# Kernel optimization log

Hardware: AMD Instinct MI355X
Metric: run time of the kernel (lower is better)

Reference implementation:

```python
import jax, jax.numpy as jnp
import numpy as np

B, T, C = 2, 4096, 768
H = 12
D = C // H  # head_dim = 64


def setup_inputs() -> dict:
    key = jax.random.key(0)
    k1, k2, k3 = jax.random.split(key, 3)
    x = jax.random.normal(k1, (B, T, C), dtype=jnp.float32)
    Wqkv = jax.random.normal(k2, (C, 3 * C), dtype=jnp.float32) * (C ** -0.5)
    Wproj = jax.random.normal(k3, (C, C), dtype=jnp.float32) * (C ** -0.5)
    bproj = jnp.zeros((C,), dtype=jnp.float32)
    return {"x": x, "Wqkv": Wqkv, "Wproj": Wproj, "bproj": bproj}


def reference(x, Wqkv, Wproj, bproj):
    b, t, c = x.shape
    # qkv projection (no bias), split into heads: [3, B, H, T, D]
    qkv = (x @ Wqkv).reshape(b, t, 3, H, D).transpose(2, 0, 3, 1, 4)
    q, k, v = qkv[0], qkv[1], qkv[2]
    scale = D ** -0.5
    # full causal score matrix [B, H, T, T] (faithful to naive impl)
    scores = jnp.einsum('bhqd,bhkd->bhqk', q, k) * scale
    causal = jnp.tril(jnp.ones((t, t), dtype=bool))
    scores = jnp.where(causal[None, None], scores, -jnp.inf)
    attn = jax.nn.softmax(scores, axis=-1)
    out = jnp.einsum('bhqk,bhkd->bhqd', attn, v)
    out = out.transpose(0, 2, 1, 3).reshape(b, t, c)
    return out @ Wproj + bproj
```

## Files before the change

### kernel.cpp

```cpp
#include <hip/hip_runtime.h>

#define B_ 2
#define T_ 4096
#define C_ 768
#define H_ 12
#define D_ 64
#define QTASK 96

typedef __attribute__((ext_vector_type(8))) short bf16x8;
typedef __attribute__((ext_vector_type(4))) float f32x4;
typedef __attribute__((ext_vector_type(16))) float f32x16;

__device__ __forceinline__ unsigned short f2bf(float f) {
  union { float f; unsigned u; } v; v.f = f;
  unsigned r = v.u + 0x7fffu + ((v.u >> 16) & 1u);
  return (unsigned short)(r >> 16);
}

__device__ __forceinline__ float exp2_hw(float x) {
  float r;
  asm("v_exp_f32 %0, %1" : "=v"(r) : "v"(x));
  return r;
}

__device__ __forceinline__ void gll16(const void* g, void* l) {
  __builtin_amdgcn_global_load_lds((const __attribute__((address_space(1))) void*)g,
                                   (__attribute__((address_space(3))) void*)l, 16, 0, 0);
}


__global__ __launch_bounds__(256) void cast_bf16_k(const float* __restrict__ in,
                                                   unsigned short* __restrict__ out, int n4,
                                                   unsigned* __restrict__ cnt) {
  int i = blockIdx.x * 256 + threadIdx.x;
  if (i < 128) cnt[i] = 0u;
  if (i >= n4) return;
  float4 v = ((const float4*)in)[i];
  union { unsigned short s[4]; unsigned long long u; } o;
  o.s[0] = f2bf(v.x); o.s[1] = f2bf(v.y); o.s[2] = f2bf(v.z); o.s[3] = f2bf(v.w);
  ((unsigned long long*)out)[i] = o.u;
}

__global__ __launch_bounds__(256) void tpose_cast_k(const float* __restrict__ in,
                                                    unsigned short* __restrict__ out,
                                                    int R, int C) {
  __shared__ unsigned short t[64][65];
  const int c0 = blockIdx.x * 64, r0 = blockIdx.y * 64;
  const int tr = threadIdx.x >> 6, tc = threadIdx.x & 63;
#pragma unroll
  for (int i = 0; i < 16; ++i) {
    int r = i * 4 + tr;
    t[r][tc] = f2bf(in[(size_t)(r0 + r) * C + c0 + tc]);
  }
  __syncthreads();
#pragma unroll
  for (int i = 0; i < 16; ++i) {
    int c = i * 4 + tr;
    out[(size_t)(c0 + c) * R + r0 + tc] = t[tc][c];
  }
}


#define QSCALE 0.1803368801111243f

template <int MODE>
__global__ __launch_bounds__(256) void gemm_k(const unsigned short* __restrict__ A,
                                              const unsigned short* __restrict__ Bt,
                                              int K,
                                              unsigned short* __restrict__ q_out,
                                              unsigned short* __restrict__ k_out,
                                              unsigned short* __restrict__ vt_out,
                                              float* __restrict__ f_out,
                                              const float* __restrict__ bias) {
  __shared__ short a_lds[2][128 * 32];
  __shared__ short b_lds[2][128 * 32];
  const int tid = threadIdx.x;
  const int wave = tid >> 6, lane = tid & 63;
  const int wm = wave >> 1, wn = wave & 1;
  const int lr = lane & 15, lc = lane >> 4;

  const int id = blockIdx.x;
  const int xcd = id & 7, idc = id >> 3;
  const int bx = xcd * 8 + (idc & 7);
  const int by = idc >> 3;
  const int m0 = bx * 128, n0 = by * 128;

  f32x4 acc[4][4];
  for (int mi = 0; mi < 4; ++mi)
    for (int ni = 0; ni < 4; ++ni) acc[mi][ni] = (f32x4){0.f, 0.f, 0.f, 0.f};

  const unsigned short *ap[2], *bp[2];
  int lb[2];
#pragma unroll
  for (int p = 0; p < 2; ++p) {
    int chunk = p * 256 + wave * 64 + lane;
    int r = chunk >> 2, cc = chunk & 3;
    int c = cc ^ ((r >> 1) & 3);
    ap[p] = A + (size_t)(m0 + r) * K + c * 8;
    bp[p] = Bt + (size_t)(n0 + r) * K + c * 8;
    lb[p] = (p * 256 + wave * 64) * 8;
  }

  const int nks = K >> 5;
#pragma unroll
  for (int p = 0; p < 2; ++p) {
    gll16(ap[p], &a_lds[0][lb[p]]);
    gll16(bp[p], &b_lds[0][lb[p]]);
    ap[p] += 32; bp[p] += 32;
  }

  for (int ks = 0; ks < nks; ++ks) {
    const int buf = ks & 1;
    __builtin_amdgcn_s_barrier();
    __builtin_amdgcn_sched_barrier(0);
    if (ks + 1 < nks) {
#pragma unroll
      for (int p = 0; p < 2; ++p) {
        gll16(ap[p], &a_lds[buf ^ 1][lb[p]]);
        gll16(bp[p], &b_lds[buf ^ 1][lb[p]]);
        ap[p] += 32; bp[p] += 32;
      }
      asm volatile("s_waitcnt vmcnt(4)" ::: "memory");
    } else {
      asm volatile("s_waitcnt vmcnt(0)" ::: "memory");
    }
    __builtin_amdgcn_sched_barrier(0);
    __builtin_amdgcn_s_barrier();
    __builtin_amdgcn_sched_barrier(0);

    bf16x8 af[4], bfrag[4];
#pragma unroll
    for (int mi = 0; mi < 4; ++mi) {
      int r = wm * 64 + mi * 16 + lr;
      af[mi] = *(const bf16x8*)&a_lds[buf][r * 32 + (lc ^ ((r >> 1) & 3)) * 8];
    }
#pragma unroll
    for (int ni = 0; ni < 4; ++ni) {
      int r = wn * 64 + ni * 16 + lr;
      bfrag[ni] = *(const bf16x8*)&b_lds[buf][r * 32 + (lc ^ ((r >> 1) & 3)) * 8];
    }
    __builtin_amdgcn_s_setprio(1);
#pragma unroll
    for (int mi = 0; mi < 4; ++mi)
#pragma unroll
      for (int ni = 0; ni < 4; ++ni)
        acc[mi][ni] = __builtin_amdgcn_mfma_f32_16x16x32_bf16(af[mi], bfrag[ni], acc[mi][ni], 0, 0, 0);
    __builtin_amdgcn_s_setprio(0);
  }

  if (MODE == 0) {
    const int nn0 = n0 + wn * 64 + lr;
    const int which = n0 / 768;
#pragma unroll
    for (int mi = 0; mi < 4; ++mi)
#pragma unroll
      for (int ni = 0; ni < 4; ++ni) {
        int nn = nn0 + ni * 16;
        int rem = nn - which * 768;
        int h = rem >> 6, d = rem & 63;
        int t0v = m0 + wm * 64 + mi * 16 + lc * 4;
        int b = t0v >> 12, t = t0v & (T_ - 1);
        size_t bh = (size_t)(b * H_ + h);
        if (which == 2) {
          unsigned u0, u1;
          asm("v_cvt_pk_bf16_f32 %0, %1, %2" : "=v"(u0) : "v"(acc[mi][ni][0]), "v"(acc[mi][ni][1]));
          asm("v_cvt_pk_bf16_f32 %0, %1, %2" : "=v"(u1) : "v"(acc[mi][ni][2]), "v"(acc[mi][ni][3]));
          uint2 u = {u0, u1};
          *(uint2*)&vt_out[(bh * D_ + d) * T_ + t] = u;
        } else {
#pragma unroll
          for (int r = 0; r < 4; ++r) {
            float av = acc[mi][ni][r];
            if (which == 0) av *= QSCALE;
            unsigned short val = f2bf(av);
            if (which == 0) q_out[(bh * T_ + t + r) * D_ + d] = val;
            else            k_out[(bh * T_ + t + r) * D_ + d] = val;
          }
        }
      }
  } else {
#pragma unroll
    for (int mi = 0; mi < 4; ++mi)
#pragma unroll
      for (int ni = 0; ni < 4; ++ni) {
        int nn = n0 + wn * 64 + ni * 16 + lr;
        float bv = bias[nn];
#pragma unroll
        for (int r = 0; r < 4; ++r) {
          int m = m0 + wm * 64 + mi * 16 + lc * 4 + r;
          f_out[(size_t)m * C_ + nn] = acc[mi][ni][r] + bv;
        }
      }
  }
}


#define PACK8(SV, O)                                                              \
  do {                                                                            \
    unsigned w0, w1, w2, w3, w4, w5, w6, w7;                                      \
    asm("v_cvt_pk_bf16_f32 %0, %1, %2" : "=v"(w0) : "v"(SV[0]), "v"(SV[1]));      \
    asm("v_cvt_pk_bf16_f32 %0, %1, %2" : "=v"(w1) : "v"(SV[2]), "v"(SV[3]));      \
    asm("v_cvt_pk_bf16_f32 %0, %1, %2" : "=v"(w2) : "v"(SV[4]), "v"(SV[5]));      \
    asm("v_cvt_pk_bf16_f32 %0, %1, %2" : "=v"(w3) : "v"(SV[6]), "v"(SV[7]));      \
    asm("v_cvt_pk_bf16_f32 %0, %1, %2" : "=v"(w4) : "v"(SV[8]), "v"(SV[9]));      \
    asm("v_cvt_pk_bf16_f32 %0, %1, %2" : "=v"(w5) : "v"(SV[10]), "v"(SV[11]));    \
    asm("v_cvt_pk_bf16_f32 %0, %1, %2" : "=v"(w6) : "v"(SV[12]), "v"(SV[13]));    \
    asm("v_cvt_pk_bf16_f32 %0, %1, %2" : "=v"(w7) : "v"(SV[14]), "v"(SV[15]));    \
    asm("v_permlane32_swap_b32 %0, %1" : "+v"(w0), "+v"(w2));                     \
    asm("v_permlane32_swap_b32 %0, %1" : "+v"(w1), "+v"(w3));                     \
    asm("v_permlane32_swap_b32 %0, %1" : "+v"(w4), "+v"(w6));                     \
    asm("v_permlane32_swap_b32 %0, %1" : "+v"(w5), "+v"(w7));                     \
    pw[(O) + 0] = w0; pw[(O) + 1] = w1; pw[(O) + 2] = w2; pw[(O) + 3] = w3;       \
    pw[(O) + 4] = w4; pw[(O) + 5] = w5; pw[(O) + 6] = w6; pw[(O) + 7] = w7;       \
  } while (0)

__global__ __launch_bounds__(256) void flash5_k(const unsigned short* __restrict__ Qg,
                                                const unsigned short* __restrict__ Kg,
                                                const unsigned short* __restrict__ Vtg,
                                                unsigned short* __restrict__ Og,
                                                unsigned* __restrict__ cnt) {
  __shared__ short k_lds[2][8 * 512];
  __shared__ short vt_lds[2][8 * 512];
  __shared__ int task_s;

  const int tid = threadIdx.x;
  const int wave = tid >> 6, lane = tid & 63;
  const int lq = lane & 31, hi = lane >> 5;
  const int xq = blockIdx.x & 7;
  unsigned* myq = cnt + xq * 16;

  for (;;) {
    if (tid == 0) task_s = (int)atomicAdd(myq, 1u);
    __syncthreads();
    const int task = task_s;
    if (task >= QTASK) return;

    const int qi = 31 - task / 3;
    const int bh = xq * 3 + (task - (task / 3) * 3);
    const int qw = qi * 128 + wave * 32;
    const int q_g = qw + lq;

    const size_t kbase = (size_t)bh * T_ * D_;
    const size_t vbase = (size_t)bh * D_ * T_;

    const unsigned short* qrow = Qg + kbase + (size_t)q_g * D_;
    bf16x8 qf[4];
#pragma unroll
    for (int t = 0; t < 4; ++t) qf[t] = *(const bf16x8*)(qrow + t * 16 + hi * 8);

    f32x16 accT0, accT1;
#pragma unroll
    for (int r = 0; r < 16; ++r) { accT0[r] = 0.f; accT1[r] = 0.f; }
    float lvec[16];
#pragma unroll
    for (int r = 0; r < 16; ++r) lvec[r] = 0.f;
    float m = 0.f;

    const int nt = 2 * qi + 2;

    const unsigned short* kp = Kg + kbase + (size_t)((wave & 1) * 32 + lq) * D_ + (wave >> 1) * 16 + hi * 8;
    const unsigned short* vp = Vtg + vbase + (size_t)((wave & 1) * 32 + lq) * T_ + (wave >> 1) * 16 + hi * 8;
    const int lb0 = wave * 512, lb1 = (wave + 4) * 512;

    gll16(kp, &k_lds[0][lb0]); gll16(kp + 32, &k_lds[0][lb1]);
    gll16(vp, &vt_lds[0][lb0]); gll16(vp + 32, &vt_lds[0][lb1]);
    const unsigned short* kpn = kp + 64 * D_;
    const unsigned short* vpn = vp + 64;

    for (int it = 0; it < nt; ++it) {
      const int kv = it * 64;
      const int buf = it & 1;

      __builtin_amdgcn_s_barrier();
      __builtin_amdgcn_sched_barrier(0);
      if (it + 1 < nt) {
        gll16(kpn, &k_lds[buf ^ 1][lb0]); gll16(kpn + 32, &k_lds[buf ^ 1][lb1]);
        gll16(vpn, &vt_lds[buf ^ 1][lb0]); gll16(vpn + 32, &vt_lds[buf ^ 1][lb1]);
        kpn += 64 * D_; vpn += 64;
        asm volatile("s_waitcnt vmcnt(4)" ::: "memory");
      } else {
        asm volatile("s_waitcnt vmcnt(0)" ::: "memory");
      }
      __builtin_amdgcn_sched_barrier(0);
      __builtin_amdgcn_s_barrier();
      __builtin_amdgcn_sched_barrier(0);

      if (kv <= qw + 31) {
        const float negm = -m;
        f32x16 s0, s1;
#pragma unroll
        for (int r = 0; r < 16; ++r) { s0[r] = negm; s1[r] = negm; }
        __builtin_amdgcn_s_setprio(1);
#pragma unroll
        for (int t = 0; t < 4; ++t) {
          bf16x8 kf0 = *(const bf16x8*)&k_lds[buf][(t * 2 + 0) * 512 + lane * 8];
          bf16x8 kf1 = *(const bf16x8*)&k_lds[buf][(t * 2 + 1) * 512 + lane * 8];
          s0 = __builtin_amdgcn_mfma_f32_32x32x16_bf16(kf0, qf[t], s0, 0, 0, 0);
          s1 = __builtin_amdgcn_mfma_f32_32x32x16_bf16(kf1, qf[t], s1, 0, 0, 0);
        }
        __builtin_amdgcn_s_setprio(0);

        if (kv + 63 > qw) {
#pragma unroll
          for (int r = 0; r < 16; ++r) {
            int key0 = kv + ((r & 3) + 8 * (r >> 2) + 4 * hi);
            if (key0 > q_g) s0[r] = -INFINITY;
            if (key0 + 32 > q_g) s1[r] = -INFINITY;
          }
        }

        float mx[16];
#pragma unroll
        for (int r = 0; r < 16; ++r) mx[r] = fmaxf(s0[r], s1[r]);
        float a0 = fmaxf(fmaxf(mx[0], mx[1]), mx[2]);
        float a1 = fmaxf(fmaxf(mx[3], mx[4]), mx[5]);
        float a2 = fmaxf(fmaxf(mx[6], mx[7]), mx[8]);
        float a3 = fmaxf(fmaxf(mx[9], mx[10]), mx[11]);
        float a4 = fmaxf(fmaxf(mx[12], mx[13]), mx[14]);
        float rx = fmaxf(fmaxf(fmaxf(a0, a1), fmaxf(a2, a3)), fmaxf(a4, mx[15]));
        rx = fmaxf(rx, __shfl_xor(rx, 32));

        if (!__all(rx <= 8.f)) {
          float dlt = fmaxf(rx, 0.f);
          float al = exp2_hw(-dlt);
          m += dlt;
#pragma unroll
          for (int r = 0; r < 16; ++r) { accT0[r] *= al; accT1[r] *= al; lvec[r] *= al; }
#pragma unroll
          for (int r = 0; r < 16; ++r) { s0[r] -= dlt; s1[r] -= dlt; }
        }
#pragma unroll
        for (int r = 0; r < 16; ++r) s0[r] = exp2_hw(s0[r]);
#pragma unroll
        for (int r = 0; r < 16; ++r) s1[r] = exp2_hw(s1[r]);
#pragma unroll
        for (int r = 0; r < 16; ++r) lvec[r] += s0[r] + s1[r];

        unsigned pw[16];
        PACK8(s0, 0);
        PACK8(s1, 8);

        __builtin_amdgcn_s_setprio(1);
#pragma unroll
        for (int ks = 0; ks < 4; ++ks) {
          union { unsigned u[4]; bf16x8 v; } pb;
          pb.u[0] = pw[ks * 4 + 0]; pb.u[1] = pw[ks * 4 + 1];
          pb.u[2] = pw[ks * 4 + 2]; pb.u[3] = pw[ks * 4 + 3];
          bf16x8 vf0 = *(const bf16x8*)&vt_lds[buf][(ks * 2 + 0) * 512 + lane * 8];
          bf16x8 vf1 = *(const bf16x8*)&vt_lds[buf][(ks * 2 + 1) * 512 + lane * 8];
          accT0 = __builtin_amdgcn_mfma_f32_32x32x16_bf16(vf0, pb.v, accT0, 0, 0, 0);
          accT1 = __builtin_amdgcn_mfma_f32_32x32x16_bf16(vf1, pb.v, accT1, 0, 0, 0);
        }
        __builtin_amdgcn_s_setprio(0);
      }
    }

    float l = 0.f;
#pragma unroll
    for (int r = 0; r < 16; ++r) l += lvec[r];
    l += __shfl_xor(l, 32);
    const float inv = 1.0f / l;
    const int b = bh / H_, h = bh - b * H_;
    unsigned short* orow = Og + ((size_t)b * T_ + q_g) * C_ + h * D_;
#pragma unroll
    for (int g = 0; g < 4; ++g) {
      int d0 = 8 * g + 4 * hi;
      float e0 = accT0[4 * g + 0] * inv, e1 = accT0[4 * g + 1] * inv;
      float e2 = accT0[4 * g + 2] * inv, e3 = accT0[4 * g + 3] * inv;
      float f0 = accT1[4 * g + 0] * inv, f1 = accT1[4 * g + 1] * inv;
      float f2 = accT1[4 * g + 2] * inv, f3 = accT1[4 * g + 3] * inv;
      uint2 ua, ub;
      asm("v_cvt_pk_bf16_f32 %0, %1, %2" : "=v"(ua.x) : "v"(e0), "v"(e1));
      asm("v_cvt_pk_bf16_f32 %0, %1, %2" : "=v"(ua.y) : "v"(e2), "v"(e3));
      asm("v_cvt_pk_bf16_f32 %0, %1, %2" : "=v"(ub.x) : "v"(f0), "v"(f1));
      asm("v_cvt_pk_bf16_f32 %0, %1, %2" : "=v"(ub.y) : "v"(f2), "v"(f3));
      *(uint2*)(orow + d0) = ua;
      *(uint2*)(orow + 32 + d0) = ub;
    }
    __syncthreads();
  }
}


extern "C" void kernel_launch(void* const* d_in, const int* in_sizes, int n_in,
                              void* d_out, int out_size, void* d_ws, size_t ws_size,
                              hipStream_t stream) {
  const float* x     = (const float*)d_in[0];
  const float* Wqkv  = (const float*)d_in[1];
  const float* Wproj = (const float*)d_in[2];
  const float* bproj = (const float*)d_in[3];
  float* out = (float*)d_out;

  char* ws = (char*)d_ws;
  unsigned short* xbf   = (unsigned short*)(ws);
  unsigned short* wqkvt = (unsigned short*)(ws + 12582912);
  unsigned short* wprjt = (unsigned short*)(ws + 16121856);
  unsigned short* Qb    = (unsigned short*)(ws + 17301504);
  unsigned short* Kb    = (unsigned short*)(ws + 29884416);
  unsigned short* Vtb   = (unsigned short*)(ws + 42467328);
  unsigned*       cnt   = (unsigned*)(ws + 55050240);

  cast_bf16_k<<<6144, 256, 0, stream>>>(x, xbf, (B_ * T_ * C_) / 4, cnt);
  tpose_cast_k<<<dim3((3 * C_) / 64, C_ / 64), 256, 0, stream>>>(Wqkv, wqkvt, C_, 3 * C_);
  tpose_cast_k<<<dim3(C_ / 64, C_ / 64), 256, 0, stream>>>(Wproj, wprjt, C_, C_);

  gemm_k<0><<<(B_ * T_ / 128) * (3 * C_ / 128), 256, 0, stream>>>(
      xbf, wqkvt, C_, Qb, Kb, Vtb, nullptr, nullptr);

  flash5_k<<<1024, 256, 0, stream>>>(Qb, Kb, Vtb, xbf, cnt);

  gemm_k<1><<<(B_ * T_ / 128) * (C_ / 128), 256, 0, stream>>>(
      xbf, wprjt, C_, nullptr, nullptr, nullptr, out, bproj);
}
```

Baseline: 197.5 us.

## Split long causal query tiles across two workgroups with ticketed partial merge

The flash-attention kernel now splits the 16 longest causal query tiles of each head into two halves along the key range. Each half is processed by a separate task. The first finisher writes bf16 partial accumulators plus its (m, l) to workspace. The second, identified by an atomic ticket, merges both with a log-sum-exp rescale and writes the output. A task table interleaves split and unsplit tiles so the work per task is more even, reducing the tail imbalance of the longest tiles. The cost is extra global traffic, an acquire/release atomic per split tile, and bf16 rounding of the partial accumulators.

```diff
diff --git a/kernel.cpp b/kernel.cpp
--- a/kernel.cpp
+++ b/kernel.cpp
@@ -5,7 +5,7 @@
 #define C_ 768
 #define H_ 12
 #define D_ 64
-#define QTASK 96
+#define QTASK 144
 
 typedef __attribute__((ext_vector_type(8))) short bf16x8;
 typedef __attribute__((ext_vector_type(4))) float f32x4;
@@ -33,7 +33,7 @@
                                                    unsigned short* __restrict__ out, int n4,
                                                    unsigned* __restrict__ cnt) {
   int i = blockIdx.x * 256 + threadIdx.x;
-  if (i < 128) cnt[i] = 0u;
+  if (i < 512) cnt[i] = 0u;
   if (i >= n4) return;
   float4 v = ((const float4*)in)[i];
   union { unsigned short s[4]; unsigned long long u; } o;
@@ -194,6 +194,25 @@
   }
 }
 
+__device__ const unsigned char g_tasktbl[48] = {
+  15, 0x80|31, 0xC0|31,
+      0x80|30, 0xC0|30,
+  14, 0x80|29, 0xC0|29,
+      0x80|28, 0xC0|28,
+  13, 0x80|27, 0xC0|27,
+      0x80|26, 0xC0|26,
+  12, 0x80|25, 0xC0|25,
+      0x80|24, 0xC0|24,
+  11, 0x80|23, 0xC0|23,
+      0x80|22, 0xC0|22,
+  10, 0x80|21, 0xC0|21,
+      0x80|20, 0xC0|20,
+   9, 0x80|19, 0xC0|19,
+      0x80|18, 0xC0|18,
+   8, 0x80|17, 0xC0|17,
+      0x80|16, 0xC0|16,
+   7, 6, 5, 4, 3, 2, 1, 0
+};
 
 #define PACK8(SV, O)                                                              \
   do {                                                                            \
@@ -214,14 +233,17 @@
     pw[(O) + 4] = w4; pw[(O) + 5] = w5; pw[(O) + 6] = w6; pw[(O) + 7] = w7;       \
   } while (0)
 
-__global__ __launch_bounds__(256) void flash5_k(const unsigned short* __restrict__ Qg,
+__global__ __launch_bounds__(256) void flash6_k(const unsigned short* __restrict__ Qg,
                                                 const unsigned short* __restrict__ Kg,
                                                 const unsigned short* __restrict__ Vtg,
                                                 unsigned short* __restrict__ Og,
-                                                unsigned* __restrict__ cnt) {
+                                                unsigned* __restrict__ cnt,
+                                                unsigned* __restrict__ tickets,
+                                                unsigned short* __restrict__ partials) {
   __shared__ short k_lds[2][8 * 512];
   __shared__ short vt_lds[2][8 * 512];
   __shared__ int task_s;
+  __shared__ int tk_s;
 
   const int tid = threadIdx.x;
   const int wave = tid >> 6, lane = tid & 63;
@@ -235,11 +257,19 @@
     const int task = task_s;
     if (task >= QTASK) return;
 
-    const int qi = 31 - task / 3;
-    const int bh = xq * 3 + (task - (task / 3) * 3);
+    const int d3 = task / 3;
+    const int desc = g_tasktbl[d3];
+    const int qi = desc & 63;
+    const int split = desc >> 7;
+    const int half = (desc >> 6) & 1;
+    const int bh = xq * 3 + (task - d3 * 3);
     const int qw = qi * 128 + wave * 32;
     const int q_g = qw + lq;
 
+    const int it0 = (split && half) ? (qi + 1) : 0;
+    const int itN = split ? (half ? (2 * qi + 2) : (qi + 1)) : (2 * qi + 2);
+    const int ntl = itN - it0;
+
     const size_t kbase = (size_t)bh * T_ * D_;
     const size_t vbase = (size_t)bh * D_ * T_;
 
@@ -256,10 +286,10 @@
     for (int r = 0; r < 16; ++r) lvec[r] = 0.f;
     float m = 0.f;
 
-    const int nt = 2 * qi + 2;
-
-    const unsigned short* kp = Kg + kbase + (size_t)((wave & 1) * 32 + lq) * D_ + (wave >> 1) * 16 + hi * 8;
-    const unsigned short* vp = Vtg + vbase + (size_t)((wave & 1) * 32 + lq) * T_ + (wave >> 1) * 16 + hi * 8;
+    const unsigned short* kp = Kg + kbase + (size_t)((wave & 1) * 32 + lq) * D_ +
+                               (wave >> 1) * 16 + hi * 8 + (size_t)it0 * 64 * D_;
+    const unsigned short* vp = Vtg + vbase + (size_t)((wave & 1) * 32 + lq) * T_ +
+                               (wave >> 1) * 16 + hi * 8 + it0 * 64;
     const int lb0 = wave * 512, lb1 = (wave + 4) * 512;
 
     gll16(kp, &k_lds[0][lb0]); gll16(kp + 32, &k_lds[0][lb1]);
@@ -267,13 +297,13 @@
     const unsigned short* kpn = kp + 64 * D_;
     const unsigned short* vpn = vp + 64;
 
-    for (int it = 0; it < nt; ++it) {
-      const int kv = it * 64;
-      const int buf = it & 1;
+    for (int j = 0; j < ntl; ++j) {
+      const int kv = (it0 + j) * 64;
+      const int buf = j & 1;
 
       __builtin_amdgcn_s_barrier();
       __builtin_amdgcn_sched_barrier(0);
-      if (it + 1 < nt) {
+      if (j + 1 < ntl) {
         gll16(kpn, &k_lds[buf ^ 1][lb0]); gll16(kpn + 32, &k_lds[buf ^ 1][lb1]);
         gll16(vpn, &vt_lds[buf ^ 1][lb0]); gll16(vpn + 32, &vt_lds[buf ^ 1][lb1]);
         kpn += 64 * D_; vpn += 64;
@@ -359,23 +389,92 @@
 #pragma unroll
     for (int r = 0; r < 16; ++r) l += lvec[r];
     l += __shfl_xor(l, 32);
-    const float inv = 1.0f / l;
-    const int b = bh / H_, h = bh - b * H_;
-    unsigned short* orow = Og + ((size_t)b * T_ + q_g) * C_ + h * D_;
-#pragma unroll
-    for (int g = 0; g < 4; ++g) {
-      int d0 = 8 * g + 4 * hi;
-      float e0 = accT0[4 * g + 0] * inv, e1 = accT0[4 * g + 1] * inv;
-      float e2 = accT0[4 * g + 2] * inv, e3 = accT0[4 * g + 3] * inv;
-      float f0 = accT1[4 * g + 0] * inv, f1 = accT1[4 * g + 1] * inv;
-      float f2 = accT1[4 * g + 2] * inv, f3 = accT1[4 * g + 3] * inv;
-      uint2 ua, ub;
-      asm("v_cvt_pk_bf16_f32 %0, %1, %2" : "=v"(ua.x) : "v"(e0), "v"(e1));
-      asm("v_cvt_pk_bf16_f32 %0, %1, %2" : "=v"(ua.y) : "v"(e2), "v"(e3));
-      asm("v_cvt_pk_bf16_f32 %0, %1, %2" : "=v"(ub.x) : "v"(f0), "v"(f1));
-      asm("v_cvt_pk_bf16_f32 %0, %1, %2" : "=v"(ub.y) : "v"(f2), "v"(f3));
-      *(uint2*)(orow + d0) = ua;
-      *(uint2*)(orow + 32 + d0) = ub;
+
+    bool do_write = true;
+    if (split) {
+      const int slot = bh * 16 + (qi - 16);
+      const int sub = slot * 2 + half;
+      unsigned short* pb = partials + (size_t)sub * 9216;
+      {
+        unsigned w[16];
+#pragma unroll
+        for (int g = 0; g < 8; ++g)
+          asm("v_cvt_pk_bf16_f32 %0, %1, %2" : "=v"(w[g]) : "v"(accT0[2 * g]), "v"(accT0[2 * g + 1]));
+#pragma unroll
+        for (int g = 0; g < 8; ++g)
+          asm("v_cvt_pk_bf16_f32 %0, %1, %2" : "=v"(w[8 + g]) : "v"(accT1[2 * g]), "v"(accT1[2 * g + 1]));
+        uint4* po = (uint4*)(pb + tid * 32);
+#pragma unroll
+        for (int g = 0; g < 4; ++g) {
+          uint4 u = {w[4 * g + 0], w[4 * g + 1], w[4 * g + 2], w[4 * g + 3]};
+          po[g] = u;
+        }
+        float2* pml = (float2*)(pb + 8192);
+        float2 ml = {m, l};
+        pml[tid] = ml;
+      }
+      __syncthreads();
+      if (tid == 0)
+        tk_s = (int)__hip_atomic_fetch_add(&tickets[slot], 1u, __ATOMIC_ACQ_REL,
+                                           __HIP_MEMORY_SCOPE_AGENT);
+      __syncthreads();
+      if (tk_s == 0) {
+        do_write = false;
+      } else {
+        const unsigned short* pb2 = partials + (size_t)(slot * 2 + (half ^ 1)) * 9216;
+        float2 oml = ((const float2*)(pb2 + 8192))[tid];
+        float newm = fmaxf(m, oml.x);
+        float se = exp2_hw(m - newm), so = exp2_hw(oml.x - newm);
+        l = l * se + oml.y * so;
+        const uint4* pv = (const uint4*)(pb2 + tid * 32);
+#pragma unroll
+        for (int g = 0; g < 2; ++g) {
+          uint4 u = pv[g];
+#pragma unroll
+          for (int e = 0; e < 4; ++e) {
+            unsigned wv = ((const unsigned*)&u)[e];
+            union { unsigned u; float f; } flo, fhi;
+            flo.u = wv << 16; fhi.u = wv & 0xffff0000u;
+            int r = g * 8 + e * 2;
+            accT0[r] = accT0[r] * se + flo.f * so;
+            accT0[r + 1] = accT0[r + 1] * se + fhi.f * so;
+          }
+        }
+#pragma unroll
+        for (int g = 0; g < 2; ++g) {
+          uint4 u = pv[2 + g];
+#pragma unroll
+          for (int e = 0; e < 4; ++e) {
+            unsigned wv = ((const unsigned*)&u)[e];
+            union { unsigned u; float f; } flo, fhi;
+            flo.u = wv << 16; fhi.u = wv & 0xffff0000u;
+            int r = g * 8 + e * 2;
+            accT1[r] = accT1[r] * se + flo.f * so;
+            accT1[r + 1] = accT1[r + 1] * se + fhi.f * so;
+          }
+        }
+      }
+    }
+
+    if (do_write) {
+      const float inv = 1.0f / l;
+      const int b = bh / H_, h = bh - b * H_;
+      unsigned short* orow = Og + ((size_t)b * T_ + q_g) * C_ + h * D_;
+#pragma unroll
+      for (int g = 0; g < 4; ++g) {
+        int d0 = 8 * g + 4 * hi;
+        float e0 = accT0[4 * g + 0] * inv, e1 = accT0[4 * g + 1] * inv;
+        float e2 = accT0[4 * g + 2] * inv, e3 = accT0[4 * g + 3] * inv;
+        float f0 = accT1[4 * g + 0] * inv, f1 = accT1[4 * g + 1] * inv;
+        float f2 = accT1[4 * g + 2] * inv, f3 = accT1[4 * g + 3] * inv;
+        uint2 ua, ub;
+        asm("v_cvt_pk_bf16_f32 %0, %1, %2" : "=v"(ua.x) : "v"(e0), "v"(e1));
+        asm("v_cvt_pk_bf16_f32 %0, %1, %2" : "=v"(ua.y) : "v"(e2), "v"(e3));
+        asm("v_cvt_pk_bf16_f32 %0, %1, %2" : "=v"(ub.x) : "v"(f0), "v"(f1));
+        asm("v_cvt_pk_bf16_f32 %0, %1, %2" : "=v"(ub.y) : "v"(f2), "v"(f3));
+        *(uint2*)(orow + d0) = ua;
+        *(uint2*)(orow + 32 + d0) = ub;
+      }
     }
     __syncthreads();
   }
@@ -399,6 +498,8 @@
   unsigned short* Kb    = (unsigned short*)(ws + 29884416);
   unsigned short* Vtb   = (unsigned short*)(ws + 42467328);
   unsigned*       cnt   = (unsigned*)(ws + 55050240);
+  unsigned*       tick  = (unsigned*)(ws + 55050240 + 512);
+  unsigned short* part  = (unsigned short*)(ws + 55052288);
 
   cast_bf16_k<<<6144, 256, 0, stream>>>(x, xbf, (B_ * T_ * C_) / 4, cnt);
   tpose_cast_k<<<dim3((3 * C_) / 64, C_ / 64), 256, 0, stream>>>(Wqkv, wqkvt, C_, 3 * C_);
@@ -407,7 +508,7 @@
   gemm_k<0><<<(B_ * T_ / 128) * (3 * C_ / 128), 256, 0, stream>>>(
       xbf, wqkvt, C_, Qb, Kb, Vtb, nullptr, nullptr);
 
-  flash5_k<<<1024, 256, 0, stream>>>(Qb, Kb, Vtb, xbf, cnt);
+  flash6_k<<<1024, 256, 0, stream>>>(Qb, Kb, Vtb, xbf, cnt, tick, part);
 
   gemm_k<1><<<(B_ * T_ / 128) * (C_ / 128), 256, 0, stream>>>(
       xbf, wprjt, C_, nullptr, nullptr, nullptr, out, bproj);
```

Measured after the change: 212.6 us. 1.08x slower.

## Replace atomic task queue flash kernel with static-grid per-wave direct-load attention

Applied to the files above, without the earlier changes.

Rewrites the attention kernel to drop the atomic work-queue and the shared LDS double-buffering. Each wave now loads its K and V fragments straight from global memory into registers and loops only over its own causal key tiles, so there are no block barriers. Blocks are statically assigned, with query tiles interleaved long and short to balance load, and occupancy is hinted at 3 blocks. The cost is that K/V reuse across the four waves now relies on cache rather than LDS, and global-load latency is no longer hidden by an explicit prefetch.

```diff
diff --git a/kernel.cpp b/kernel.cpp
--- a/kernel.cpp
+++ b/kernel.cpp
@@ -5,7 +5,6 @@
 #define C_ 768
 #define H_ 12
 #define D_ 64
-#define QTASK 96
 
 typedef __attribute__((ext_vector_type(8))) short bf16x8;
 typedef __attribute__((ext_vector_type(4))) float f32x4;
@@ -30,10 +29,8 @@
 
 
 __global__ __launch_bounds__(256) void cast_bf16_k(const float* __restrict__ in,
-                                                   unsigned short* __restrict__ out, int n4,
-                                                   unsigned* __restrict__ cnt) {
+                                                   unsigned short* __restrict__ out, int n4) {
   int i = blockIdx.x * 256 + threadIdx.x;
-  if (i < 128) cnt[i] = 0u;
   if (i >= n4) return;
   float4 v = ((const float4*)in)[i];
   union { unsigned short s[4]; unsigned long long u; } o;
@@ -214,170 +211,144 @@
     pw[(O) + 4] = w4; pw[(O) + 5] = w5; pw[(O) + 6] = w6; pw[(O) + 7] = w7;       \
   } while (0)
 
-__global__ __launch_bounds__(256) void flash5_k(const unsigned short* __restrict__ Qg,
-                                                const unsigned short* __restrict__ Kg,
-                                                const unsigned short* __restrict__ Vtg,
-                                                unsigned short* __restrict__ Og,
-                                                unsigned* __restrict__ cnt) {
-  __shared__ short k_lds[2][8 * 512];
-  __shared__ short vt_lds[2][8 * 512];
-  __shared__ int task_s;
-
+__global__ __launch_bounds__(256, 3) void flash7_k(const unsigned short* __restrict__ Qg,
+                                                   const unsigned short* __restrict__ Kg,
+                                                   const unsigned short* __restrict__ Vtg,
+                                                   unsigned short* __restrict__ Og) {
   const int tid = threadIdx.x;
   const int wave = tid >> 6, lane = tid & 63;
   const int lq = lane & 31, hi = lane >> 5;
-  const int xq = blockIdx.x & 7;
-  unsigned* myq = cnt + xq * 16;
-
-  for (;;) {
-    if (tid == 0) task_s = (int)atomicAdd(myq, 1u);
-    __syncthreads();
-    const int task = task_s;
-    if (task >= QTASK) return;
-
-    const int qi = 31 - task / 3;
-    const int bh = xq * 3 + (task - (task / 3) * 3);
-    const int qw = qi * 128 + wave * 32;
-    const int q_g = qw + lq;
-
-    const size_t kbase = (size_t)bh * T_ * D_;
-    const size_t vbase = (size_t)bh * D_ * T_;
-
-    const unsigned short* qrow = Qg + kbase + (size_t)q_g * D_;
-    bf16x8 qf[4];
-#pragma unroll
-    for (int t = 0; t < 4; ++t) qf[t] = *(const bf16x8*)(qrow + t * 16 + hi * 8);
-
-    f32x16 accT0, accT1;
-#pragma unroll
-    for (int r = 0; r < 16; ++r) { accT0[r] = 0.f; accT1[r] = 0.f; }
-    float lvec[16];
-#pragma unroll
-    for (int r = 0; r < 16; ++r) lvec[r] = 0.f;
-    float m = 0.f;
-
-    const int nt = 2 * qi + 2;
-
-    const unsigned short* kp = Kg + kbase + (size_t)((wave & 1) * 32 + lq) * D_ + (wave >> 1) * 16 + hi * 8;
-    const unsigned short* vp = Vtg + vbase + (size_t)((wave & 1) * 32 + lq) * T_ + (wave >> 1) * 16 + hi * 8;
-    const int lb0 = wave * 512, lb1 = (wave + 4) * 512;
-
-    gll16(kp, &k_lds[0][lb0]); gll16(kp + 32, &k_lds[0][lb1]);
-    gll16(vp, &vt_lds[0][lb0]); gll16(vp + 32, &vt_lds[0][lb1]);
-    const unsigned short* kpn = kp + 64 * D_;
-    const unsigned short* vpn = vp + 64;
-
-    for (int it = 0; it < nt; ++it) {
-      const int kv = it * 64;
-      const int buf = it & 1;
-
-      __builtin_amdgcn_s_barrier();
-      __builtin_amdgcn_sched_barrier(0);
-      if (it + 1 < nt) {
-        gll16(kpn, &k_lds[buf ^ 1][lb0]); gll16(kpn + 32, &k_lds[buf ^ 1][lb1]);
-        gll16(vpn, &vt_lds[buf ^ 1][lb0]); gll16(vpn + 32, &vt_lds[buf ^ 1][lb1]);
-        kpn += 64 * D_; vpn += 64;
-        asm volatile("s_waitcnt vmcnt(4)" ::: "memory");
-      } else {
-        asm volatile("s_waitcnt vmcnt(0)" ::: "memory");
+
+  const int bid = blockIdx.x;
+  const int xcd = bid & 7, j = bid >> 3;
+  const int g = j / 3, rb = j - g * 3;
+  const int bh = xcd * 3 + rb;
+  const int qi = (g & 1) ? (g >> 1) : (31 - (g >> 1));
+
+  const int qw = qi * 128 + wave * 32;
+  const int q_g = qw + lq;
+  const int ntw = (qw >> 6) + 1;
+
+  const size_t kbase = (size_t)bh * T_ * D_;
+  const size_t vbase = (size_t)bh * D_ * T_;
+
+  const unsigned short* qrow = Qg + kbase + (size_t)q_g * D_;
+  bf16x8 qf[4];
+#pragma unroll
+  for (int t = 0; t < 4; ++t) qf[t] = *(const bf16x8*)(qrow + t * 16 + hi * 8);
+
+  f32x16 accT0, accT1;
+#pragma unroll
+  for (int r = 0; r < 16; ++r) { accT0[r] = 0.f; accT1[r] = 0.f; }
+  float lvec[8];
+#pragma unroll
+  for (int r = 0; r < 8; ++r) lvec[r] = 0.f;
+  float m = 0.f;
+
+  const unsigned short* kp0 = Kg + kbase + (size_t)lq * D_ + hi * 8;
+  const unsigned short* vp0 = Vtg + vbase + (size_t)lq * T_ + hi * 8;
+
+  for (int it = 0; it < ntw; ++it) {
+    const int kv = it * 64;
+    const unsigned short* kp = kp0 + (size_t)kv * D_;
+    const unsigned short* vp = vp0 + kv;
+
+    bf16x8 kf[8], vf[8];
+#pragma unroll
+    for (int t = 0; t < 4; ++t) {
+      kf[2 * t]     = *(const bf16x8*)(kp + t * 16);
+      kf[2 * t + 1] = *(const bf16x8*)(kp + 32 * D_ + t * 16);
+      vf[2 * t]     = *(const bf16x8*)(vp + t * 16);
+      vf[2 * t + 1] = *(const bf16x8*)(vp + (size_t)32 * T_ + t * 16);
+    }
+
+    const float negm = -m;
+    f32x16 s0, s1;
+#pragma unroll
+    for (int r = 0; r < 16; ++r) { s0[r] = negm; s1[r] = negm; }
+    __builtin_amdgcn_s_setprio(1);
+#pragma unroll
+    for (int t = 0; t < 4; ++t) {
+      s0 = __builtin_amdgcn_mfma_f32_32x32x16_bf16(kf[2 * t], qf[t], s0, 0, 0, 0);
+      s1 = __builtin_amdgcn_mfma_f32_32x32x16_bf16(kf[2 * t + 1], qf[t], s1, 0, 0, 0);
+    }
+    __builtin_amdgcn_s_setprio(0);
+
+    if (kv + 63 > qw) {
+#pragma unroll
+      for (int r = 0; r < 16; ++r) {
+        int key0 = kv + ((r & 3) + 8 * (r >> 2) + 4 * hi);
+        if (key0 > q_g) s0[r] = -INFINITY;
+        if (key0 + 32 > q_g) s1[r] = -INFINITY;
       }
-      __builtin_amdgcn_sched_barrier(0);
-      __builtin_amdgcn_s_barrier();
-      __builtin_amdgcn_sched_barrier(0);
-
-      if (kv <= qw + 31) {
-        const float negm = -m;
-        f32x16 s0, s1;
-#pragma unroll
-        for (int r = 0; r < 16; ++r) { s0[r] = negm; s1[r] = negm; }
-        __builtin_amdgcn_s_setprio(1);
-#pragma unroll
-        for (int t = 0; t < 4; ++t) {
-          bf16x8 kf0 = *(const bf16x8*)&k_lds[buf][(t * 2 + 0) * 512 + lane * 8];
-          bf16x8 kf1 = *(const bf16x8*)&k_lds[buf][(t * 2 + 1) * 512 + lane * 8];
-          s0 = __builtin_amdgcn_mfma_f32_32x32x16_bf16(kf0, qf[t], s0, 0, 0, 0);
-          s1 = __builtin_amdgcn_mfma_f32_32x32x16_bf16(kf1, qf[t], s1, 0, 0, 0);
-        }
-        __builtin_amdgcn_s_setprio(0);
-
-        if (kv + 63 > qw) {
-#pragma unroll
-          for (int r = 0; r < 16; ++r) {
-            int key0 = kv + ((r & 3) + 8 * (r >> 2) + 4 * hi);
-            if (key0 > q_g) s0[r] = -INFINITY;
-            if (key0 + 32 > q_g) s1[r] = -INFINITY;
-          }
-        }
-
-        float mx[16];
-#pragma unroll
-        for (int r = 0; r < 16; ++r) mx[r] = fmaxf(s0[r], s1[r]);
-        float a0 = fmaxf(fmaxf(mx[0], mx[1]), mx[2]);
-        float a1 = fmaxf(fmaxf(mx[3], mx[4]), mx[5]);
-        float a2 = fmaxf(fmaxf(mx[6], mx[7]), mx[8]);
-        float a3 = fmaxf(fmaxf(mx[9], mx[10]), mx[11]);
-        float a4 = fmaxf(fmaxf(mx[12], mx[13]), mx[14]);
-        float rx = fmaxf(fmaxf(fmaxf(a0, a1), fmaxf(a2, a3)), fmaxf(a4, mx[15]));
-        rx = fmaxf(rx, __shfl_xor(rx, 32));
-
-        if (!__all(rx <= 8.f)) {
-          float dlt = fmaxf(rx, 0.f);
-          float al = exp2_hw(-dlt);
-          m += dlt;
-#pragma unroll
-          for (int r = 0; r < 16; ++r) { accT0[r] *= al; accT1[r] *= al; lvec[r] *= al; }
-#pragma unroll
-          for (int r = 0; r < 16; ++r) { s0[r] -= dlt; s1[r] -= dlt; }
-        }
-#pragma unroll
-        for (int r = 0; r < 16; ++r) s0[r] = exp2_hw(s0[r]);
-#pragma unroll
-        for (int r = 0; r < 16; ++r) s1[r] = exp2_hw(s1[r]);
-#pragma unroll
-        for (int r = 0; r < 16; ++r) lvec[r] += s0[r] + s1[r];
-
-        unsigned pw[16];
-        PACK8(s0, 0);
-        PACK8(s1, 8);
-
-        __builtin_amdgcn_s_setprio(1);
-#pragma unroll
-        for (int ks = 0; ks < 4; ++ks) {
-          union { unsigned u[4]; bf16x8 v; } pb;
-          pb.u[0] = pw[ks * 4 + 0]; pb.u[1] = pw[ks * 4 + 1];
-          pb.u[2] = pw[ks * 4 + 2]; pb.u[3] = pw[ks * 4 + 3];
-          bf16x8 vf0 = *(const bf16x8*)&vt_lds[buf][(ks * 2 + 0) * 512 + lane * 8];
-          bf16x8 vf1 = *(const bf16x8*)&vt_lds[buf][(ks * 2 + 1) * 512 + lane * 8];
-          accT0 = __builtin_amdgcn_mfma_f32_32x32x16_bf16(vf0, pb.v, accT0, 0, 0, 0);
-          accT1 = __builtin_amdgcn_mfma_f32_32x32x16_bf16(vf1, pb.v, accT1, 0, 0, 0);
-        }
-        __builtin_amdgcn_s_setprio(0);
-      }
-    }
-
-    float l = 0.f;
-#pragma unroll
-    for (int r = 0; r < 16; ++r) l += lvec[r];
-    l += __shfl_xor(l, 32);
-    const float inv = 1.0f / l;
-    const int b = bh / H_, h = bh - b * H_;
-    unsigned short* orow = Og + ((size_t)b * T_ + q_g) * C_ + h * D_;
-#pragma unroll
-    for (int g = 0; g < 4; ++g) {
-      int d0 = 8 * g + 4 * hi;
-      float e0 = accT0[4 * g + 0] * inv, e1 = accT0[4 * g + 1] * inv;
-      float e2 = accT0[4 * g + 2] * inv, e3 = accT0[4 * g + 3] * inv;
-      float f0 = accT1[4 * g + 0] * inv, f1 = accT1[4 * g + 1] * inv;
-      float f2 = accT1[4 * g + 2] * inv, f3 = accT1[4 * g + 3] * inv;
-      uint2 ua, ub;
-      asm("v_cvt_pk_bf16_f32 %0, %1, %2" : "=v"(ua.x) : "v"(e0), "v"(e1));
-      asm("v_cvt_pk_bf16_f32 %0, %1, %2" : "=v"(ua.y) : "v"(e2), "v"(e3));
-      asm("v_cvt_pk_bf16_f32 %0, %1, %2" : "=v"(ub.x) : "v"(f0), "v"(f1));
-      asm("v_cvt_pk_bf16_f32 %0, %1, %2" : "=v"(ub.y) : "v"(f2), "v"(f3));
-      *(uint2*)(orow + d0) = ua;
-      *(uint2*)(orow + 32 + d0) = ub;
-    }
-    __syncthreads();
+    }
+
+    float mx[16];
+#pragma unroll
+    for (int r = 0; r < 16; ++r) mx[r] = fmaxf(s0[r], s1[r]);
+    float a0 = fmaxf(fmaxf(mx[0], mx[1]), mx[2]);
+    float a1 = fmaxf(fmaxf(mx[3], mx[4]), mx[5]);
+    float a2 = fmaxf(fmaxf(mx[6], mx[7]), mx[8]);
+    float a3 = fmaxf(fmaxf(mx[9], mx[10]), mx[11]);
+    float a4 = fmaxf(fmaxf(mx[12], mx[13]), mx[14]);
+    float rx = fmaxf(fmaxf(fmaxf(a0, a1), fmaxf(a2, a3)), fmaxf(a4, mx[15]));
+    rx = fmaxf(rx, __shfl_xor(rx, 32));
+
+    if (!__all(rx <= 8.f)) {
+      float dlt = fmaxf(rx, 0.f);
+      float al = exp2_hw(-dlt);
+      m += dlt;
+#pragma unroll
+      for (int r = 0; r < 16; ++r) { accT0[r] *= al; accT1[r] *= al; }
+#pragma unroll
+      for (int r = 0; r < 8; ++r) lvec[r] *= al;
+#pragma unroll
+      for (int r = 0; r < 16; ++r) { s0[r] -= dlt; s1[r] -= dlt; }
+    }
+#pragma unroll
+    for (int r = 0; r < 16; ++r) s0[r] = exp2_hw(s0[r]);
+#pragma unroll
+    for (int r = 0; r < 16; ++r) s1[r] = exp2_hw(s1[r]);
+#pragma unroll
+    for (int r = 0; r < 8; ++r) lvec[r] += (s0[r] + s1[r]) + (s0[r + 8] + s1[r + 8]);
+
+    unsigned pw[16];
+    PACK8(s0, 0);
+    PACK8(s1, 8);
+
+    __builtin_amdgcn_s_setprio(1);
+#pragma unroll
+    for (int ks = 0; ks < 4; ++ks) {
+      union { unsigned u[4]; bf16x8 v; } pb;
+      pb.u[0] = pw[ks * 4 + 0]; pb.u[1] = pw[ks * 4 + 1];
+      pb.u[2] = pw[ks * 4 + 2]; pb.u[3] = pw[ks * 4 + 3];
+      accT0 = __builtin_amdgcn_mfma_f32_32x32x16_bf16(vf[2 * ks], pb.v, accT0, 0, 0, 0);
+      accT1 = __builtin_amdgcn_mfma_f32_32x32x16_bf16(vf[2 * ks + 1], pb.v, accT1, 0, 0, 0);
+    }
+    __builtin_amdgcn_s_setprio(0);
+  }
+
+  float l = 0.f;
+#pragma unroll
+  for (int r = 0; r < 8; ++r) l += lvec[r];
+  l += __shfl_xor(l, 32);
+  const float inv = 1.0f / l;
+  const int b = bh / H_, h = bh - b * H_;
+  unsigned short* orow = Og + ((size_t)b * T_ + q_g) * C_ + h * D_;
+#pragma unroll
+  for (int gg = 0; gg < 4; ++gg) {
+    int d0 = 8 * gg + 4 * hi;
+    float e0 = accT0[4 * gg + 0] * inv, e1 = accT0[4 * gg + 1] * inv;
+    float e2 = accT0[4 * gg + 2] * inv, e3 = accT0[4 * gg + 3] * inv;
+    float f0 = accT1[4 * gg + 0] * inv, f1 = accT1[4 * gg + 1] * inv;
+    float f2 = accT1[4 * gg + 2] * inv, f3 = accT1[4 * gg + 3] * inv;
+    uint2 ua, ub;
+    asm("v_cvt_pk_bf16_f32 %0, %1, %2" : "=v"(ua.x) : "v"(e0), "v"(e1));
+    asm("v_cvt_pk_bf16_f32 %0, %1, %2" : "=v"(ua.y) : "v"(e2), "v"(e3));
+    asm("v_cvt_pk_bf16_f32 %0, %1, %2" : "=v"(ub.x) : "v"(f0), "v"(f1));
+    asm("v_cvt_pk_bf16_f32 %0, %1, %2" : "=v"(ub.y) : "v"(f2), "v"(f3));
+    *(uint2*)(orow + d0) = ua;
+    *(uint2*)(orow + 32 + d0) = ub;
   }
 }
 
@@ -398,16 +369,15 @@
   unsigned short* Qb    = (unsigned short*)(ws + 17301504);
   unsigned short* Kb    = (unsigned short*)(ws + 29884416);
   unsigned short* Vtb   = (unsigned short*)(ws + 42467328);
-  unsigned*       cnt   = (unsigned*)(ws + 55050240);
-
-  cast_bf16_k<<<6144, 256, 0, stream>>>(x, xbf, (B_ * T_ * C_) / 4, cnt);
+
+  cast_bf16_k<<<6144, 256, 0, stream>>>(x, xbf, (B_ * T_ * C_) / 4);
   tpose_cast_k<<<dim3((3 * C_) / 64, C_ / 64), 256, 0, stream>>>(Wqkv, wqkvt, C_, 3 * C_);
   tpose_cast_k<<<dim3(C_ / 64, C_ / 64), 256, 0, stream>>>(Wproj, wprjt, C_, C_);
 
   gemm_k<0><<<(B_ * T_ / 128) * (3 * C_ / 128), 256, 0, stream>>>(
       xbf, wqkvt, C_, Qb, Kb, Vtb, nullptr, nullptr);
 
-  flash5_k<<<1024, 256, 0, stream>>>(Qb, Kb, Vtb, xbf, cnt);
+  flash7_k<<<768, 256, 0, stream>>>(Qb, Kb, Vtb, xbf);
 
   gemm_k<1><<<(B_ * T_ / 128) * (C_ / 128), 256, 0, stream>>>(
       xbf, wprjt, C_, nullptr, nullptr, nullptr, out, bproj);
```

New measurement: 329.4 us. +66.8%, slower.

## Triple-buffer K/V tiles in flash attention and halve persistent grid

Applied to the files above, without the earlier changes.

The K and V^T LDS staging moves from a double buffer to a triple buffer, prefetching two tiles ahead with matching vmcnt waits so global loads have more time to land before use. The row-sum accumulator shrinks from 16 to 8 registers by pairing partial sums, cutting register use and add work. The persistent grid drops from 1024 to 512 blocks, which affects how many workers pull tasks from the atomic queues. The extra buffer raises LDS use per block, which can lower occupancy.

```diff
diff --git a/kernel.cpp b/kernel.cpp
--- a/kernel.cpp
+++ b/kernel.cpp
@@ -214,13 +214,13 @@
     pw[(O) + 4] = w4; pw[(O) + 5] = w5; pw[(O) + 6] = w6; pw[(O) + 7] = w7;       \
   } while (0)
 
-__global__ __launch_bounds__(256) void flash5_k(const unsigned short* __restrict__ Qg,
+__global__ __launch_bounds__(256) void flash8_k(const unsigned short* __restrict__ Qg,
                                                 const unsigned short* __restrict__ Kg,
                                                 const unsigned short* __restrict__ Vtg,
                                                 unsigned short* __restrict__ Og,
                                                 unsigned* __restrict__ cnt) {
-  __shared__ short k_lds[2][8 * 512];
-  __shared__ short vt_lds[2][8 * 512];
+  __shared__ short k_lds[3][8 * 512];
+  __shared__ short vt_lds[3][8 * 512];
   __shared__ int task_s;
 
   const int tid = threadIdx.x;
@@ -251,32 +251,40 @@
     f32x16 accT0, accT1;
 #pragma unroll
     for (int r = 0; r < 16; ++r) { accT0[r] = 0.f; accT1[r] = 0.f; }
-    float lvec[16];
-#pragma unroll
-    for (int r = 0; r < 16; ++r) lvec[r] = 0.f;
+    float lvec[8];
+#pragma unroll
+    for (int r = 0; r < 8; ++r) lvec[r] = 0.f;
     float m = 0.f;
 
-    const int nt = 2 * qi + 2;
-
-    const unsigned short* kp = Kg + kbase + (size_t)((wave & 1) * 32 + lq) * D_ + (wave >> 1) * 16 + hi * 8;
-    const unsigned short* vp = Vtg + vbase + (size_t)((wave & 1) * 32 + lq) * T_ + (wave >> 1) * 16 + hi * 8;
+    const int ntl = 2 * qi + 2;
+
+    const unsigned short* kp0 = Kg + kbase + (size_t)((wave & 1) * 32 + lq) * D_ +
+                                (wave >> 1) * 16 + hi * 8;
+    const unsigned short* vp0 = Vtg + vbase + (size_t)((wave & 1) * 32 + lq) * T_ +
+                                (wave >> 1) * 16 + hi * 8;
     const int lb0 = wave * 512, lb1 = (wave + 4) * 512;
 
-    gll16(kp, &k_lds[0][lb0]); gll16(kp + 32, &k_lds[0][lb1]);
-    gll16(vp, &vt_lds[0][lb0]); gll16(vp + 32, &vt_lds[0][lb1]);
-    const unsigned short* kpn = kp + 64 * D_;
-    const unsigned short* vpn = vp + 64;
-
-    for (int it = 0; it < nt; ++it) {
-      const int kv = it * 64;
-      const int buf = it & 1;
+    auto stage = [&](int it, int sb) {
+      const unsigned short* kp = kp0 + (size_t)it * 64 * D_;
+      const unsigned short* vp = vp0 + it * 64;
+      gll16(kp, &k_lds[sb][lb0]); gll16(kp + 32, &k_lds[sb][lb1]);
+      gll16(vp, &vt_lds[sb][lb0]); gll16(vp + 32, &vt_lds[sb][lb1]);
+    };
+
+    stage(0, 0);
+    stage(1, 1);
+
+    int buf = 0;
+    for (int j = 0; j < ntl; ++j) {
+      const int kv = j * 64;
 
       __builtin_amdgcn_s_barrier();
       __builtin_amdgcn_sched_barrier(0);
-      if (it + 1 < nt) {
-        gll16(kpn, &k_lds[buf ^ 1][lb0]); gll16(kpn + 32, &k_lds[buf ^ 1][lb1]);
-        gll16(vpn, &vt_lds[buf ^ 1][lb0]); gll16(vpn + 32, &vt_lds[buf ^ 1][lb1]);
-        kpn += 64 * D_; vpn += 64;
+      if (j + 2 < ntl) {
+        int tb = buf + 2; if (tb >= 3) tb -= 3;
+        stage(j + 2, tb);
+        asm volatile("s_waitcnt vmcnt(8)" ::: "memory");
+      } else if (j + 1 < ntl) {
         asm volatile("s_waitcnt vmcnt(4)" ::: "memory");
       } else {
         asm volatile("s_waitcnt vmcnt(0)" ::: "memory");
@@ -325,7 +333,9 @@
           float al = exp2_hw(-dlt);
           m += dlt;
 #pragma unroll
-          for (int r = 0; r < 16; ++r) { accT0[r] *= al; accT1[r] *= al; lvec[r] *= al; }
+          for (int r = 0; r < 16; ++r) { accT0[r] *= al; accT1[r] *= al; }
+#pragma unroll
+          for (int r = 0; r < 8; ++r) lvec[r] *= al;
 #pragma unroll
           for (int r = 0; r < 16; ++r) { s0[r] -= dlt; s1[r] -= dlt; }
         }
@@ -334,7 +344,7 @@
 #pragma unroll
         for (int r = 0; r < 16; ++r) s1[r] = exp2_hw(s1[r]);
 #pragma unroll
-        for (int r = 0; r < 16; ++r) lvec[r] += s0[r] + s1[r];
+        for (int r = 0; r < 8; ++r) lvec[r] += (s0[r] + s1[r]) + (s0[r + 8] + s1[r + 8]);
 
         unsigned pw[16];
         PACK8(s0, 0);
@@ -353,11 +363,12 @@
         }
         __builtin_amdgcn_s_setprio(0);
       }
+      ++buf; if (buf >= 3) buf = 0;
     }
 
     float l = 0.f;
 #pragma unroll
-    for (int r = 0; r < 16; ++r) l += lvec[r];
+    for (int r = 0; r < 8; ++r) l += lvec[r];
     l += __shfl_xor(l, 32);
     const float inv = 1.0f / l;
     const int b = bh / H_, h = bh - b * H_;
@@ -407,7 +418,7 @@
   gemm_k<0><<<(B_ * T_ / 128) * (3 * C_ / 128), 256, 0, stream>>>(
       xbf, wqkvt, C_, Qb, Kb, Vtb, nullptr, nullptr);
 
-  flash5_k<<<1024, 256, 0, stream>>>(Qb, Kb, Vtb, xbf, cnt);
+  flash8_k<<<512, 256, 0, stream>>>(Qb, Kb, Vtb, xbf, cnt);
 
   gemm_k<1><<<(B_ * T_ / 128) * (C_ / 128), 256, 0, stream>>>(
       xbf, wprjt, C_, nullptr, nullptr, nullptr, out, bproj);
```

Measured after the change: 200.6 us. Within noise of the previous version (+1.6%).
